# Optimization experiments

Measured on AMD Instinct MI355X. Metric: run time of the kernel, lower is better.

The kernel has to match this reference:

```python
import jax, jax.numpy as jnp
import numpy as np
from jax import lax

CTX = 768  # ctx_len from the module globals


def _causal_grouped_conv(sig, w):
    # sig: [B,C,L], w: [C,K] -> [B,C,L]; torch F.conv1d(groups=C) with left pad K-1
    # (cross-correlation semantics, same as lax.conv_general_dilated)
    K = w.shape[-1]
    return lax.conv_general_dilated(
        sig, w[:, None, :], (1,), [(K - 1, 0)],
        feature_group_count=sig.shape[1],
        dimension_numbers=("NCH", "OIH", "NCH"))


def setup_inputs() -> dict:
    key = jax.random.key(0)
    ks = jax.random.split(key, 10)
    B, T, C = 8, 767, 1024
    s = 1.0 / np.sqrt(C).astype(np.float32)
    return {
        "x": jax.random.normal(ks[0], (B, T, C), jnp.float32),
        "xx": jax.random.normal(ks[1], (B, C), jnp.float32),          # prev-token state
        "aa": jax.random.uniform(ks[2], (B, C), jnp.float32),          # wkv numerator carry
        "bb": jax.random.uniform(ks[3], (B, C), jnp.float32) + 0.5,    # wkv denominator carry (>0)
        "mm": jnp.zeros((B, C), jnp.float32),                          # prev power-of-two normalizer (log-ish)
        "time_decay": jax.random.normal(ks[4], (C, 1), jnp.float32) * 0.1,
        "time_first": jnp.full((C, 1), np.log(0.3), jnp.float32),
        "time_mix": jax.random.uniform(ks[5], (1, 1, C), jnp.float32),
        "Wk": jax.random.normal(ks[6], (C, C), jnp.float32) * s,
        "Wv": jax.random.normal(ks[7], (C, C), jnp.float32) * s,
        "Wr": jax.random.normal(ks[8], (C, C), jnp.float32) * s,
        "Wo": jax.random.normal(ks[9], (C, C), jnp.float32) * s,
    }


def reference(x, xx, aa, bb, mm, time_decay, time_first, time_mix, Wk, Wv, Wr, Wo):
    B, T, C = x.shape
    # time_shift: prepend carried last-token features, drop last
    x_prev = jnp.concatenate([xx[:, None, :], x[:, :-1, :]], axis=1)
    xm = x * time_mix + x_prev * (1.0 - time_mix)
    k = jnp.einsum('btc,dc->bdt', xm, Wk)  # [B,C,T]
    v = jnp.einsum('btc,dc->bdt', xm, Wv)
    r = jnp.einsum('btc,dc->btd', xm, Wr)  # [B,T,C]
    # power-of-two normalizer via frexp/ldexp (no grad path, exponent is int)
    m = jnp.max(k, axis=-1)                                  # [B,C]
    _, expn = jnp.frexp(lax.stop_gradient(m))
    mm_new = jnp.ldexp(jnp.asarray(0.5, k.dtype), expn)      # 0.5 * 2**exp
    k = jnp.exp(k - mm_new[..., None])
    kv = k * v
    # decay kernel: time_curve = [-(CTX-2)..0], last column = exp(time_first)
    time_curve = -(CTX - 2.0 - jnp.arange(CTX - 1, dtype=x.dtype))
    w_full = jnp.exp(jnp.concatenate(
        [jnp.exp(time_decay) * time_curve[None, :], time_first], axis=-1))  # [C,CTX]
    # carry-in columns rescaled to new normalizer
    rsf = jnp.exp(mm - mm_new)                               # [B,C]
    k_ext = jnp.concatenate([(bb * rsf)[..., None], k], axis=-1)    # [B,C,T+1]
    kv_ext = jnp.concatenate([(aa * rsf)[..., None], kv], axis=-1)  # [B,C,T+1]
    w = w_full[:, -(T + 1):]                                 # [C,T+1]
    wkv = _causal_grouped_conv(kv_ext, w)[..., 1:]           # [B,C,T]
    wk = _causal_grouped_conv(k_ext, w)[..., 1:]             # [B,C,T]
    rwkv = jax.nn.sigmoid(r) * jnp.nan_to_num(wkv / wk).transpose(0, 2, 1)  # [B,T,C]
    return jnp.einsum('btc,dc->btd', rwkv, Wo)
```

## Files before the change

### kernel.cpp

```cpp
#include <hip/hip_runtime.h>
#include <float.h>


typedef __bf16 bf16x8 __attribute__((ext_vector_type(8)));
typedef __bf16 bf16x4 __attribute__((ext_vector_type(4)));
typedef float  f32x4  __attribute__((ext_vector_type(4)));

#define NCH 32

#define GLOAD_LDS16(g, l)                                                  \
  __builtin_amdgcn_global_load_lds(                                       \
      (__attribute__((address_space(1))) void*)(g),                       \
      (__attribute__((address_space(3))) void*)(l), 16, 0, 0)

__global__ __launch_bounds__(256)
void xm_split_kernel(const float* __restrict__ x, const float* __restrict__ xx,
                     const float* __restrict__ tmix,
                     __bf16* __restrict__ xh, __bf16* __restrict__ xl,
                     int B, int T, int C, int Mpad) {
  long i4 = (long)blockIdx.x * 256 + threadIdx.x;
  long tot = (long)Mpad * C / 4;
  if (i4 >= tot) return;
  long flat = i4 * 4;
  int c = (int)(flat % C);
  long m = flat / C;
  float4 o;
  if (m >= (long)B * T) {
    o = make_float4(0.f, 0.f, 0.f, 0.f);
  } else {
    int t = (int)(m % T);
    int b = (int)(m / T);
    float4 xv = *(const float4*)&x[flat];
    float4 tm = *(const float4*)&tmix[c];
    float4 pv;
    if (t == 0) pv = *(const float4*)&xx[(long)b * C + c];
    else        pv = *(const float4*)&x[flat - C];
    o.x = xv.x * tm.x + pv.x * (1.0f - tm.x);
    o.y = xv.y * tm.y + pv.y * (1.0f - tm.y);
    o.z = xv.z * tm.z + pv.z * (1.0f - tm.z);
    o.w = xv.w * tm.w + pv.w * (1.0f - tm.w);
  }
  bf16x4 hv, lv;
  hv[0] = (__bf16)o.x; lv[0] = (__bf16)(o.x - (float)hv[0]);
  hv[1] = (__bf16)o.y; lv[1] = (__bf16)(o.y - (float)hv[1]);
  hv[2] = (__bf16)o.z; lv[2] = (__bf16)(o.z - (float)hv[2]);
  hv[3] = (__bf16)o.w; lv[3] = (__bf16)(o.w - (float)hv[3]);
  *(bf16x4*)&xh[flat] = hv;
  *(bf16x4*)&xl[flat] = lv;
}

__global__ __launch_bounds__(256)
void w_split_kernel(const float* __restrict__ W0, const float* __restrict__ W1,
                    const float* __restrict__ W2, const float* __restrict__ W3,
                    __bf16* __restrict__ wh, __bf16* __restrict__ wl, long CC) {
  int z = blockIdx.y;
  const float* __restrict__ W = (z == 0) ? W0 : (z == 1) ? W1 : (z == 2) ? W2 : W3;
  long i4 = (long)blockIdx.x * 256 + threadIdx.x;
  if (i4 * 4 >= CC) return;
  long flat = i4 * 4;
  float4 v = *(const float4*)&W[flat];
  bf16x4 hv, lv;
  hv[0] = (__bf16)v.x; lv[0] = (__bf16)(v.x - (float)hv[0]);
  hv[1] = (__bf16)v.y; lv[1] = (__bf16)(v.y - (float)hv[1]);
  hv[2] = (__bf16)v.z; lv[2] = (__bf16)(v.z - (float)hv[2]);
  hv[3] = (__bf16)v.w; lv[3] = (__bf16)(v.w - (float)hv[3]);
  *(bf16x4*)&wh[z * CC + flat] = hv;
  *(bf16x4*)&wl[z * CC + flat] = lv;
}

__global__ __launch_bounds__(256)
void gemm_split(const __bf16* __restrict__ Xh, const __bf16* __restrict__ Xl,
                const __bf16* __restrict__ Wh, const __bf16* __restrict__ Wl,
                float* __restrict__ O0, float* __restrict__ O1,
                float* __restrict__ O2, int M, int N, int K) {
  const int z = blockIdx.z;
  const __bf16* __restrict__ Bh = Wh + (size_t)z * N * K;
  const __bf16* __restrict__ Bl = Wl + (size_t)z * N * K;
  float* __restrict__ O = (z == 0) ? O0 : (z == 1) ? O1 : O2;

  __shared__ __bf16 sAh[128 * 32];
  __shared__ __bf16 sAl[128 * 32];
  __shared__ __bf16 sBh[128 * 32];
  __shared__ __bf16 sBl[128 * 32];

  const int tid  = threadIdx.x;
  const int wid  = tid >> 6;
  const int lane = tid & 63;
  const int bm = blockIdx.x * 128;
  const int bn = blockIdx.y * 128;
  const int wrow = wid >> 1;
  const int wcol = wid & 1;

  f32x4 acc[4][4] = {};

  const int srow = lane >> 2;
  const int scu  = lane & 3;

  for (int k0 = 0; k0 < K; k0 += 32) {
    __syncthreads();
    #pragma unroll
    for (int i = 0; i < 2; ++i) {
      const int rb0 = wid * 32 + i * 16;
      const size_t ga = (size_t)(bm + rb0 + srow) * K + k0 + scu * 8;
      const size_t gb = (size_t)(bn + rb0 + srow) * K + k0 + scu * 8;
      const int lo = rb0 * 32;
      GLOAD_LDS16(&Xh[ga], &sAh[lo]);
      GLOAD_LDS16(&Xl[ga], &sAl[lo]);
      GLOAD_LDS16(&Bh[gb], &sBh[lo]);
      GLOAD_LDS16(&Bl[gb], &sBl[lo]);
    }
    __syncthreads();

    const int lrow = lane & 15;
    const int lk   = (lane >> 4) * 8;
    bf16x8 ah[4], al[4], bh[4], bl[4];
    #pragma unroll
    for (int m = 0; m < 4; ++m) {
      const int r = (wrow * 64 + m * 16 + lrow) * 32 + lk;
      ah[m] = *(const bf16x8*)&sAh[r];
      al[m] = *(const bf16x8*)&sAl[r];
    }
    #pragma unroll
    for (int n = 0; n < 4; ++n) {
      const int r = (wcol * 64 + n * 16 + lrow) * 32 + lk;
      bh[n] = *(const bf16x8*)&sBh[r];
      bl[n] = *(const bf16x8*)&sBl[r];
    }
    #pragma unroll
    for (int m = 0; m < 4; ++m)
      #pragma unroll
      for (int n = 0; n < 4; ++n) {
        acc[m][n] = __builtin_amdgcn_mfma_f32_16x16x32_bf16(ah[m], bh[n], acc[m][n], 0, 0, 0);
        acc[m][n] = __builtin_amdgcn_mfma_f32_16x16x32_bf16(ah[m], bl[n], acc[m][n], 0, 0, 0);
        acc[m][n] = __builtin_amdgcn_mfma_f32_16x16x32_bf16(al[m], bh[n], acc[m][n], 0, 0, 0);
      }
  }

  const int crow = (lane >> 4) * 4;
  const int ccol = lane & 15;
  #pragma unroll
  for (int m = 0; m < 4; ++m)
    #pragma unroll
    for (int n = 0; n < 4; ++n) {
      const int gn = bn + wcol * 64 + n * 16 + ccol;
      #pragma unroll
      for (int i = 0; i < 4; ++i) {
        const int gm = bm + wrow * 64 + m * 16 + crow + i;
        if (gm < M) O[(size_t)gm * N + gn] = acc[m][n][i];
      }
    }
}

__global__ __launch_bounds__(256)
void scan_pass1(float* __restrict__ kbuf, float* __restrict__ vbuf,
                const float* __restrict__ td,
                float* __restrict__ P, float* __restrict__ Skv,
                float* __restrict__ Sk, int B, int T, int C, int L) {
  int g = blockIdx.x * 256 + threadIdx.x;
  int j = blockIdx.y;
  int b = g / C, c = g % C;
  float etd = expf(td[c]);
  float decay = expf(-etd);
  int t0 = j * L, t1 = min(T, t0 + L);
  float skv = 0.0f, sk = 0.0f;
  size_t base = (size_t)b * T * C + c;
  #pragma unroll 4
  for (int t = t0; t < t1; ++t) {
    size_t idx = base + (size_t)t * C;
    float kk = expf(kbuf[idx]);
    float kv = kk * vbuf[idx];
    kbuf[idx] = kk;
    vbuf[idx] = kv;
    skv = fmaf(decay, skv, kv);
    sk  = fmaf(decay, sk, kk);
  }
  size_t o = (size_t)j * (B * C) + g;
  P[o] = expf(-etd * (float)(t1 - t0));
  Skv[o] = skv; Sk[o] = sk;
}

__global__ __launch_bounds__(256)
void scan_combine(const float* __restrict__ P, const float* __restrict__ Skv,
                  const float* __restrict__ Sk, const float* __restrict__ aa,
                  const float* __restrict__ bb, const float* __restrict__ mm,
                  float* __restrict__ A0kv, float* __restrict__ A0k, int BC) {
  int g = blockIdx.x * 256 + threadIdx.x;
  if (g >= BC) return;
  float rsf = expf(mm[g]);
  float A = aa[g] * rsf;
  float Bst = bb[g] * rsf;
  #pragma unroll
  for (int j = 0; j < NCH; ++j) {
    size_t o = (size_t)j * BC + g;
    float p = P[o], skv = Skv[o], sk = Sk[o];
    A0kv[o] = A; A0k[o] = Bst;
    A   = fmaf(p, A, skv);
    Bst = fmaf(p, Bst, sk);
  }
}

__global__ __launch_bounds__(256)
void scan_pass2(const float* __restrict__ kbuf, const float* __restrict__ vbuf,
                const float* __restrict__ rbuf, const float* __restrict__ td,
                const float* __restrict__ tf, const float* __restrict__ A0kv,
                const float* __restrict__ A0k,
                __bf16* __restrict__ oh, __bf16* __restrict__ ol,
                int B, int T, int C, int L) {
  int g = blockIdx.x * 256 + threadIdx.x;
  int j = blockIdx.y;
  int b = g / C, c = g % C;
  float decay = expf(-expf(td[c]));
  float tfe = expf(tf[c]);
  size_t o = (size_t)j * (B * C) + g;
  float A = A0kv[o];
  float Bst = A0k[o];
  int t0 = j * L, t1 = min(T, t0 + L);
  size_t base = (size_t)b * T * C + c;
  #pragma unroll 4
  for (int t = t0; t < t1; ++t) {
    size_t idx = base + (size_t)t * C;
    float kk = kbuf[idx];
    float kv = vbuf[idx];
    float rr = rbuf[idx];
    float wkv = fmaf(kv, tfe, A);
    float wk  = fmaf(kk, tfe, Bst);
    float q = wkv / wk;
    if (isnan(q)) q = 0.0f;
    else if (isinf(q)) q = (q > 0.0f) ? FLT_MAX : -FLT_MAX;
    float sig = 1.0f / (1.0f + expf(-rr));
    float val = sig * q;
    __bf16 h = (__bf16)val;
    oh[idx] = h;
    ol[idx] = (__bf16)(val - (float)h);
    A   = fmaf(decay, A, kv);
    Bst = fmaf(decay, Bst, kk);
  }
}

extern "C" void kernel_launch(void* const* d_in, const int* in_sizes, int n_in,
                              void* d_out, int out_size, void* d_ws, size_t ws_size,
                              hipStream_t stream) {
  const float* x    = (const float*)d_in[0];
  const float* xx   = (const float*)d_in[1];
  const float* aa   = (const float*)d_in[2];
  const float* bb   = (const float*)d_in[3];
  const float* mm   = (const float*)d_in[4];
  const float* td   = (const float*)d_in[5];
  const float* tf   = (const float*)d_in[6];
  const float* tmix = (const float*)d_in[7];
  const float* Wk   = (const float*)d_in[8];
  const float* Wv   = (const float*)d_in[9];
  const float* Wr   = (const float*)d_in[10];
  const float* Wo   = (const float*)d_in[11];
  float* out = (float*)d_out;

  const int C = in_sizes[5];
  const int B = in_sizes[1] / C;
  const int T = in_sizes[0] / (B * C);
  const int M = B * T;
  const int Mpad = ((M + 127) / 128) * 128;
  const int BC = B * C;
  const long CC = (long)C * C;
  const int L = (T + NCH - 1) / NCH;

  char* p = (char*)d_ws;
  __bf16* xh = (__bf16*)p;  p += (size_t)Mpad * C * 2;
  __bf16* xl = (__bf16*)p;  p += (size_t)Mpad * C * 2;
  __bf16* wh = (__bf16*)p;  p += (size_t)4 * CC * 2;
  __bf16* wl = (__bf16*)p;  p += (size_t)4 * CC * 2;
  float* kb  = (float*)p;   p += (size_t)M * C * 4;
  float* vb  = (float*)p;   p += (size_t)M * C * 4;
  float* rb  = (float*)p;   p += (size_t)M * C * 4;
  float* Pb   = (float*)(wh);
  float* Skv  = (float*)(wh + CC);
  float* Sk   = (float*)(wh + 2 * CC);
  float* A0kv = (float*)(wl);
  float* A0k  = (float*)(wl + CC);
  __bf16* rh = xh;
  __bf16* rl = xl;

  long nf4 = (long)Mpad * C / 4;
  xm_split_kernel<<<dim3((unsigned)((nf4 + 255) / 256)), 256, 0, stream>>>(
      x, xx, tmix, xh, xl, B, T, C, Mpad);

  w_split_kernel<<<dim3((unsigned)(CC / 4 / 256), 4), 256, 0, stream>>>(
      Wk, Wv, Wr, Wo, wh, wl, CC);

  dim3 g3(Mpad / 128, C / 128, 3);
  gemm_split<<<g3, 256, 0, stream>>>(xh, xl, wh, wl, kb, vb, rb, M, C, C);

  scan_pass1<<<dim3(BC / 256, NCH), 256, 0, stream>>>(kb, vb, td, Pb, Skv, Sk,
                                                      B, T, C, L);
  scan_combine<<<dim3(BC / 256), 256, 0, stream>>>(Pb, Skv, Sk, aa, bb, mm,
                                                   A0kv, A0k, BC);
  scan_pass2<<<dim3(BC / 256, NCH), 256, 0, stream>>>(kb, vb, rb, td, tf,
                                                      A0kv, A0k, rh, rl,
                                                      B, T, C, L);

  dim3 g1(Mpad / 128, C / 128, 1);
  gemm_split<<<g1, 256, 0, stream>>>(rh, rl, wh + 3 * CC, wl + 3 * CC,
                                     out, out, out, M, C, C);
}
```

Before: 323.2 us.

## Drop low-order MFMA for r GEMM, recompute exp in pass2, smaller final GEMM tiles

In the r projection (z==2) the GEMM skips the al*bh correction MFMA, since r only feeds a sigmoid and needs less precision. scan_pass1 no longer writes exp(k) and k*v back to global memory, and scan_pass2 recomputes them from the raw buffers, cutting memory writes at the cost of extra exp work. The output GEMM moves to a new 64x128 tile kernel, giving twice as many blocks for better occupancy across CUs. The r change lowers sigmoid-input precision slightly.

Measured after the change: 347.4 us. +7.5%, slower.

```diff
diff --git a/kernel.cpp b/kernel.cpp
--- a/kernel.cpp
+++ b/kernel.cpp
@@ -132,7 +132,8 @@
       for (int n = 0; n < 4; ++n) {
         acc[m][n] = __builtin_amdgcn_mfma_f32_16x16x32_bf16(ah[m], bh[n], acc[m][n], 0, 0, 0);
         acc[m][n] = __builtin_amdgcn_mfma_f32_16x16x32_bf16(ah[m], bl[n], acc[m][n], 0, 0, 0);
-        acc[m][n] = __builtin_amdgcn_mfma_f32_16x16x32_bf16(al[m], bh[n], acc[m][n], 0, 0, 0);
+        if (z != 2)
+          acc[m][n] = __builtin_amdgcn_mfma_f32_16x16x32_bf16(al[m], bh[n], acc[m][n], 0, 0, 0);
       }
   }
 
@@ -152,7 +153,86 @@
 }
 
 __global__ __launch_bounds__(256)
-void scan_pass1(float* __restrict__ kbuf, float* __restrict__ vbuf,
+void gemm_fin(const __bf16* __restrict__ Xh, const __bf16* __restrict__ Xl,
+              const __bf16* __restrict__ Wh, const __bf16* __restrict__ Wl,
+              float* __restrict__ O, int M, int N, int K) {
+  __shared__ __bf16 sAh[64 * 32];
+  __shared__ __bf16 sAl[64 * 32];
+  __shared__ __bf16 sBh[128 * 32];
+  __shared__ __bf16 sBl[128 * 32];
+
+  const int tid  = threadIdx.x;
+  const int wid  = tid >> 6;
+  const int lane = tid & 63;
+  const int bm = blockIdx.x * 64;
+  const int bn = blockIdx.y * 128;
+  const int wrow = wid >> 1;
+  const int wcol = wid & 1;
+
+  f32x4 acc[2][4] = {};
+
+  const int srow = lane >> 2;
+  const int scu  = lane & 3;
+
+  for (int k0 = 0; k0 < K; k0 += 32) {
+    __syncthreads();
+    {
+      const int rb0 = wid * 16;
+      const size_t ga = (size_t)(bm + rb0 + srow) * K + k0 + scu * 8;
+      GLOAD_LDS16(&Xh[ga], &sAh[rb0 * 32]);
+      GLOAD_LDS16(&Xl[ga], &sAl[rb0 * 32]);
+    }
+    #pragma unroll
+    for (int i = 0; i < 2; ++i) {
+      const int rb0 = wid * 32 + i * 16;
+      const size_t gb = (size_t)(bn + rb0 + srow) * K + k0 + scu * 8;
+      GLOAD_LDS16(&Wh[gb], &sBh[rb0 * 32]);
+      GLOAD_LDS16(&Wl[gb], &sBl[rb0 * 32]);
+    }
+    __syncthreads();
+
+    const int lrow = lane & 15;
+    const int lk   = (lane >> 4) * 8;
+    bf16x8 ah[2], al[2], bh[4], bl[4];
+    #pragma unroll
+    for (int m = 0; m < 2; ++m) {
+      const int r = (wrow * 32 + m * 16 + lrow) * 32 + lk;
+      ah[m] = *(const bf16x8*)&sAh[r];
+      al[m] = *(const bf16x8*)&sAl[r];
+    }
+    #pragma unroll
+    for (int n = 0; n < 4; ++n) {
+      const int r = (wcol * 64 + n * 16 + lrow) * 32 + lk;
+      bh[n] = *(const bf16x8*)&sBh[r];
+      bl[n] = *(const bf16x8*)&sBl[r];
+    }
+    #pragma unroll
+    for (int m = 0; m < 2; ++m)
+      #pragma unroll
+      for (int n = 0; n < 4; ++n) {
+        acc[m][n] = __builtin_amdgcn_mfma_f32_16x16x32_bf16(ah[m], bh[n], acc[m][n], 0, 0, 0);
+        acc[m][n] = __builtin_amdgcn_mfma_f32_16x16x32_bf16(ah[m], bl[n], acc[m][n], 0, 0, 0);
+        acc[m][n] = __builtin_amdgcn_mfma_f32_16x16x32_bf16(al[m], bh[n], acc[m][n], 0, 0, 0);
+      }
+  }
+
+  const int crow = (lane >> 4) * 4;
+  const int ccol = lane & 15;
+  #pragma unroll
+  for (int m = 0; m < 2; ++m)
+    #pragma unroll
+    for (int n = 0; n < 4; ++n) {
+      const int gn = bn + wcol * 64 + n * 16 + ccol;
+      #pragma unroll
+      for (int i = 0; i < 4; ++i) {
+        const int gm = bm + wrow * 32 + m * 16 + crow + i;
+        if (gm < M) O[(size_t)gm * N + gn] = acc[m][n][i];
+      }
+    }
+}
+
+__global__ __launch_bounds__(256)
+void scan_pass1(const float* __restrict__ kbuf, const float* __restrict__ vbuf,
                 const float* __restrict__ td,
                 float* __restrict__ P, float* __restrict__ Skv,
                 float* __restrict__ Sk, int B, int T, int C, int L) {
@@ -169,8 +249,6 @@
     size_t idx = base + (size_t)t * C;
     float kk = expf(kbuf[idx]);
     float kv = kk * vbuf[idx];
-    kbuf[idx] = kk;
-    vbuf[idx] = kv;
     skv = fmaf(decay, skv, kv);
     sk  = fmaf(decay, sk, kk);
   }
@@ -219,9 +297,11 @@
   #pragma unroll 4
   for (int t = t0; t < t1; ++t) {
     size_t idx = base + (size_t)t * C;
-    float kk = kbuf[idx];
-    float kv = vbuf[idx];
+    float kr = kbuf[idx];
+    float vv = vbuf[idx];
     float rr = rbuf[idx];
+    float kk = expf(kr);
+    float kv = kk * vv;
     float wkv = fmaf(kv, tfe, A);
     float wk  = fmaf(kk, tfe, Bst);
     float q = wkv / wk;
@@ -297,7 +377,7 @@
                                                       A0kv, A0k, rh, rl,
                                                       B, T, C, L);
 
-  dim3 g1(Mpad / 128, C / 128, 1);
-  gemm_split<<<g1, 256, 0, stream>>>(rh, rl, wh + 3 * CC, wl + 3 * CC,
-                                     out, out, out, M, C, C);
-}
+  dim3 gf(Mpad / 64, C / 128);
+  gemm_fin<<<gf, 256, 0, stream>>>(rh, rl, wh + 3 * CC, wl + 3 * CC,
+                                   out, M, C, C);
+}
```
